# Performance work log

Measured on AMD Instinct MI355X. Metric: run time of the kernel, lower is better.

Reference implementation:

```python
import jax, jax.numpy as jnp
import numpy as np

EPS = 1e-5

def _layer_norm(x, w, b):
    m = jnp.mean(x, axis=-1, keepdims=True)
    v = jnp.var(x, axis=-1, keepdims=True)
    return (x - m) * jax.lax.rsqrt(v + EPS) * w + b


def setup_inputs() -> dict:
    key = jax.random.key(0)
    ks = jax.random.split(key, 8)
    N, L, c_s, c_z, H, d = 2, 512, 384, 128, 12, 32
    w_scale = 0.05  # keep logits in a numerically sane range
    return {
        "s": jax.random.normal(ks[0], (N, L, c_s), jnp.float32),
        "z": jax.random.normal(ks[1], (N, L, L, c_z), jnp.float32),
        "ln_s_w": jnp.ones((c_s,), jnp.float32),
        "ln_s_b": jnp.zeros((c_s,), jnp.float32),
        "ln_z_w": jnp.ones((c_z,), jnp.float32),
        "ln_z_b": jnp.zeros((c_z,), jnp.float32),
        "wz": jax.random.normal(ks[2], (H, c_z), jnp.float32) * w_scale,
        "wq": jax.random.normal(ks[3], (c_s, H, d), jnp.float32) * w_scale,
        "wk": jax.random.normal(ks[4], (c_s, H, d), jnp.float32) * w_scale,
        "wv": jax.random.normal(ks[5], (c_s, H, d), jnp.float32) * w_scale,
        "wg": jax.random.normal(ks[6], (c_s, H, d), jnp.float32) * w_scale,
        "bg": jnp.ones((H, d), jnp.float32),
        "wo": jax.random.normal(ks[7], (H, d, c_s), jnp.float32) * w_scale,
        "bo": jnp.zeros((c_s,), jnp.float32),
    }


def reference(s, z, ln_s_w, ln_s_b, ln_z_w, ln_z_b, wz, wq, wk, wv, wg, bg, wo, bo):
    d = wq.shape[-1]
    s_n = _layer_norm(s, ln_s_w, ln_s_b)            # [N,L,c_s]
    z_n = _layer_norm(z, ln_z_w, ln_z_b)            # [N,L,L,c_z]
    bias = jnp.einsum('nijc,hc->nhij', z_n, wz)     # [N,H,L,L] per-head pair bias
    q = jnp.einsum('nlc,chd->nhld', s_n, wq) * (1.0 / jnp.sqrt(jnp.asarray(d, s.dtype)))
    k = jnp.einsum('nlc,chd->nhld', s_n, wk)
    v = jnp.einsum('nlc,chd->nhld', s_n, wv)
    logits = jnp.einsum('nhid,nhjd->nhij', q, k) + bias
    attn = jax.nn.softmax(logits, axis=-1)
    o = jnp.einsum('nhij,nhjd->nihd', attn, v)      # [N,L,H,d]
    g = jax.nn.sigmoid(jnp.einsum('nlc,chd->nlhd', s_n, wg) + bg)
    o = o * g
    out = jnp.einsum('nlhd,hdc->nlc', o, wo) + bo   # [N,L,c_s]
    return out
```

## Files before the change

### kernel.cpp

```cpp
#include <hip/hip_runtime.h>
#include <math.h>

#define N_  2
#define L_  512
#define CS  384
#define CZ  128
#define H_  12
#define D_  32
#define HD  384

__device__ __forceinline__ float sigmoidf_(float x) { return 1.f / (1.f + __expf(-x)); }

__global__ __launch_bounds__(64) void k_ln_s(const float* __restrict__ s,
        const float* __restrict__ w, const float* __restrict__ b,
        float* __restrict__ sn) {
    int row = blockIdx.x;
    const float* x = s + (size_t)row * CS;
    float* y = sn + (size_t)row * CS;
    int lane = threadIdx.x;
    float v[6];
    float sum = 0.f, sq = 0.f;
#pragma unroll
    for (int e = 0; e < 6; ++e) {
        v[e] = x[lane + e * 64];
        sum += v[e];
        sq  += v[e] * v[e];
    }
#pragma unroll
    for (int o = 1; o < 64; o <<= 1) {
        sum += __shfl_xor(sum, o);
        sq  += __shfl_xor(sq , o);
    }
    float m = sum * (1.f / CS);
    float var = sq * (1.f / CS) - m * m;
    float rstd = rsqrtf(var + 1e-5f);
#pragma unroll
    for (int e = 0; e < 6; ++e) {
        int c = lane + e * 64;
        y[c] = (v[e] - m) * rstd * w[c] + b[c];
    }
}

__global__ __launch_bounds__(128) void k_wz_prep(const float* __restrict__ lnzw,
        const float* __restrict__ lnzb, const float* __restrict__ wz,
        float* __restrict__ wzp, float* __restrict__ wzps, float* __restrict__ wzb) {
    __shared__ float sp[H_][CZ];
    __shared__ float sb[H_][CZ];
    int c = threadIdx.x;
    float lw = lnzw[c], lb = lnzb[c];
    for (int h = 0; h < H_; ++h) {
        float w = wz[h * CZ + c];
        float p = lw * w;
        sp[h][c] = p;
        sb[h][c] = lb * w;
        wzp[h * CZ + c] = p;
    }
    __syncthreads();
    if (c < H_) {
        float s1 = 0.f, s2 = 0.f;
        for (int e = 0; e < CZ; ++e) { s1 += sp[c][e]; s2 += sb[c][e]; }
        wzps[c] = s1; wzb[c] = s2;
    }
}

__global__ __launch_bounds__(384) void k_proj(const float* __restrict__ sn,
        const float* __restrict__ wq, const float* __restrict__ wk,
        const float* __restrict__ wv, const float* __restrict__ wg,
        float* __restrict__ q, float* __restrict__ k, float* __restrict__ v,
        float* __restrict__ g) {
    __shared__ float s_lds[8][CS];
    int t = threadIdx.x;
    int row0 = blockIdx.x * 8;
    {
        const float4* src = (const float4*)(sn + (size_t)row0 * CS);
        float4* dst = (float4*)(&s_lds[0][0]);
        dst[t] = src[t];
        dst[t + 384] = src[t + 384];
    }
    __syncthreads();
    int mat = t / 96;
    int col = (t % 96) * 4;
    const float* W = (mat == 0) ? wq : (mat == 1) ? wk : (mat == 2) ? wv : wg;
    float acc[8][4];
#pragma unroll
    for (int r = 0; r < 8; ++r)
#pragma unroll
        for (int j = 0; j < 4; ++j) acc[r][j] = 0.f;
    for (int kk = 0; kk < CS; kk += 4) {
        float4 w0 = *(const float4*)(W + (size_t)(kk + 0) * HD + col);
        float4 w1 = *(const float4*)(W + (size_t)(kk + 1) * HD + col);
        float4 w2 = *(const float4*)(W + (size_t)(kk + 2) * HD + col);
        float4 w3 = *(const float4*)(W + (size_t)(kk + 3) * HD + col);
#pragma unroll
        for (int r = 0; r < 8; ++r) {
            float4 sv = *(const float4*)(&s_lds[r][kk]);
            acc[r][0] += sv.x * w0.x + sv.y * w1.x + sv.z * w2.x + sv.w * w3.x;
            acc[r][1] += sv.x * w0.y + sv.y * w1.y + sv.z * w2.y + sv.w * w3.y;
            acc[r][2] += sv.x * w0.z + sv.y * w1.z + sv.z * w2.z + sv.w * w3.z;
            acc[r][3] += sv.x * w0.w + sv.y * w1.w + sv.z * w2.w + sv.w * w3.w;
        }
    }
    float* out = (mat == 0) ? q : (mat == 1) ? k : (mat == 2) ? v : g;
    float scale = (mat == 0) ? 0.17677669529663687f : 1.f;
#pragma unroll
    for (int r = 0; r < 8; ++r) {
        float4 o;
        o.x = acc[r][0] * scale; o.y = acc[r][1] * scale;
        o.z = acc[r][2] * scale; o.w = acc[r][3] * scale;
        *(float4*)(out + (size_t)(row0 + r) * HD + col) = o;
    }
}

__global__ __launch_bounds__(384) void k_bias(const float* __restrict__ z,
        const float* __restrict__ wzp, const float* __restrict__ wzps,
        const float* __restrict__ wzb, float* __restrict__ bias) {
    __shared__ float z_lds[32][132];
    __shared__ float w_lds[H_][132];
    __shared__ float m_lds[32], r_lds[32];
    __shared__ float ws_lds[H_], wb_lds[H_];
    int t = threadIdx.x;
    int jt = blockIdx.x, i = blockIdx.y, n = blockIdx.z;
    int j0 = jt * 32;
    {
        int h = t >> 5, c4 = t & 31;
        *(float4*)(&w_lds[h][c4 * 4]) = *(const float4*)(wzp + h * CZ + c4 * 4);
        if (t < H_) { ws_lds[t] = wzps[t]; wb_lds[t] = wzb[t]; }
    }
    {
        const float4* src = (const float4*)(z + ((size_t)(n * L_ + i) * L_ + j0) * CZ);
        int idx = t;
        *(float4*)(&z_lds[idx >> 5][(idx & 31) * 4]) = src[idx];
        idx = t + 384;
        *(float4*)(&z_lds[idx >> 5][(idx & 31) * 4]) = src[idx];
        if (t < 256) {
            idx = t + 768;
            *(float4*)(&z_lds[idx >> 5][(idx & 31) * 4]) = src[idx];
        }
    }
    __syncthreads();
    if (t < 256) {
        int r = t >> 3, lane = t & 7;
        float s1 = 0.f, s2 = 0.f;
#pragma unroll
        for (int e4 = 0; e4 < 4; ++e4) {
            float4 v = *(const float4*)(&z_lds[r][lane * 16 + e4 * 4]);
            s1 += v.x + v.y + v.z + v.w;
            s2 += v.x * v.x + v.y * v.y + v.z * v.z + v.w * v.w;
        }
#pragma unroll
        for (int o = 1; o < 8; o <<= 1) { s1 += __shfl_xor(s1, o); s2 += __shfl_xor(s2, o); }
        if (lane == 0) {
            float m = s1 * (1.f / CZ);
            float var = s2 * (1.f / CZ) - m * m;
            m_lds[r] = m;
            r_lds[r] = rsqrtf(var + 1e-5f);
        }
    }
    __syncthreads();
    int h = t >> 5, j = t & 31;
    float acc = 0.f;
#pragma unroll 8
    for (int c4 = 0; c4 < 32; ++c4) {
        float4 zv = *(const float4*)(&z_lds[j][c4 * 4]);
        float4 wv = *(const float4*)(&w_lds[h][c4 * 4]);
        acc += zv.x * wv.x + zv.y * wv.y + zv.z * wv.z + zv.w * wv.w;
    }
    float bv = r_lds[j] * (acc - m_lds[j] * ws_lds[h]) + wb_lds[h];
    bias[(((size_t)n * H_ + h) * L_ + i) * L_ + j0 + j] = bv;
}

__global__ __launch_bounds__(256) void k_attn(const float* __restrict__ q,
        const float* __restrict__ k, const float* __restrict__ v,
        const float* __restrict__ gpre, const float* __restrict__ bg,
        const float* __restrict__ bias, float* __restrict__ og) {
    __shared__ float p_lds[16][516];
    __shared__ float k_lds[64][36];
    __shared__ float rinv[16];
    int t = threadIdx.x;
    int it = blockIdx.x, h = blockIdx.y, n = blockIdx.z;
    int i0 = it * 16;
    int i = t >> 4, jsub = t & 15;
    float4 qr[8];
    const float* qrow = q + ((size_t)(n * L_) + i0 + i) * HD + h * D_;
#pragma unroll
    for (int d4 = 0; d4 < 8; ++d4) qr[d4] = *(const float4*)(qrow + d4 * 4);
    const float* bias_row = bias + (((size_t)n * H_ + h) * L_ + i0 + i) * L_;

    for (int s = 0; s < 8; ++s) {
        const float* kbase = k + (size_t)(n * L_ + s * 64) * HD + h * D_;
        {
            int idx = t;
            *(float4*)(&k_lds[idx >> 3][(idx & 7) * 4]) =
                *(const float4*)(kbase + (size_t)(idx >> 3) * HD + (idx & 7) * 4);
            idx = t + 256;
            *(float4*)(&k_lds[idx >> 3][(idx & 7) * 4]) =
                *(const float4*)(kbase + (size_t)(idx >> 3) * HD + (idx & 7) * 4);
        }
        __syncthreads();
        float acc[4];
#pragma unroll
        for (int jj = 0; jj < 4; ++jj) acc[jj] = bias_row[s * 64 + jsub + jj * 16];
#pragma unroll
        for (int d4 = 0; d4 < 8; ++d4) {
            float4 qv = qr[d4];
#pragma unroll
            for (int jj = 0; jj < 4; ++jj) {
                float4 kv = *(const float4*)(&k_lds[jsub + jj * 16][d4 * 4]);
                acc[jj] += qv.x * kv.x + qv.y * kv.y + qv.z * kv.z + qv.w * kv.w;
            }
        }
#pragma unroll
        for (int jj = 0; jj < 4; ++jj) p_lds[i][s * 64 + jsub + jj * 16] = acc[jj];
        __syncthreads();
    }
    {
        float mx = -1e30f;
#pragma unroll
        for (int e = 0; e < 8; ++e) {
            float4 x = *(const float4*)(&p_lds[i][jsub * 32 + e * 4]);
            mx = fmaxf(mx, fmaxf(fmaxf(x.x, x.y), fmaxf(x.z, x.w)));
        }
#pragma unroll
        for (int o = 1; o < 16; o <<= 1) mx = fmaxf(mx, __shfl_xor(mx, o));
        float sum = 0.f;
#pragma unroll
        for (int e = 0; e < 8; ++e) {
            float4 x = *(const float4*)(&p_lds[i][jsub * 32 + e * 4]);
            x.x = __expf(x.x - mx); x.y = __expf(x.y - mx);
            x.z = __expf(x.z - mx); x.w = __expf(x.w - mx);
            *(float4*)(&p_lds[i][jsub * 32 + e * 4]) = x;
            sum += x.x + x.y + x.z + x.w;
        }
#pragma unroll
        for (int o = 1; o < 16; o <<= 1) sum += __shfl_xor(sum, o);
        if (jsub == 0) rinv[i] = 1.f / sum;
    }
    __syncthreads();
    {
        int d = jsub * 2;
        const float* vcol = v + (size_t)(n * L_) * HD + h * D_ + d;
        float o0 = 0.f, o1 = 0.f;
        for (int j = 0; j < L_; ++j) {
            float2 vv = *(const float2*)(vcol + (size_t)j * HD);
            float p = p_lds[i][j];
            o0 += p * vv.x; o1 += p * vv.y;
        }
        float ri = rinv[i];
        o0 *= ri; o1 *= ri;
        size_t gidx = ((size_t)(n * L_) + i0 + i) * HD + h * D_ + d;
        float g0 = sigmoidf_(gpre[gidx]     + bg[h * D_ + d]);
        float g1 = sigmoidf_(gpre[gidx + 1] + bg[h * D_ + d + 1]);
        og[gidx]     = o0 * g0;
        og[gidx + 1] = o1 * g1;
    }
}

__global__ __launch_bounds__(384) void k_out(const float* __restrict__ og,
        const float* __restrict__ wo, const float* __restrict__ bo,
        float* __restrict__ out) {
    __shared__ float o_lds[8][HD];
    int t = threadIdx.x;
    int row0 = blockIdx.x * 8;
    {
        const float4* src = (const float4*)(og + (size_t)row0 * HD);
        float4* dst = (float4*)(&o_lds[0][0]);
        dst[t] = src[t];
        dst[t + 384] = src[t + 384];
    }
    __syncthreads();
    float acc[8];
#pragma unroll
    for (int r = 0; r < 8; ++r) acc[r] = 0.f;
    for (int kk = 0; kk < HD; kk += 4) {
        float w0 = wo[(size_t)(kk + 0) * CS + t];
        float w1 = wo[(size_t)(kk + 1) * CS + t];
        float w2 = wo[(size_t)(kk + 2) * CS + t];
        float w3 = wo[(size_t)(kk + 3) * CS + t];
#pragma unroll
        for (int r = 0; r < 8; ++r) {
            float4 ov = *(const float4*)(&o_lds[r][kk]);
            acc[r] += ov.x * w0 + ov.y * w1 + ov.z * w2 + ov.w * w3;
        }
    }
    float bv = bo[t];
#pragma unroll
    for (int r = 0; r < 8; ++r) out[(size_t)(row0 + r) * CS + t] = acc[r] + bv;
}

extern "C" void kernel_launch(void* const* d_in, const int* in_sizes, int n_in,
                              void* d_out, int out_size, void* d_ws, size_t ws_size,
                              hipStream_t stream) {
    const float* s    = (const float*)d_in[0];
    const float* z    = (const float*)d_in[1];
    const float* lnsw = (const float*)d_in[2];
    const float* lnsb = (const float*)d_in[3];
    const float* lnzw = (const float*)d_in[4];
    const float* lnzb = (const float*)d_in[5];
    const float* wz   = (const float*)d_in[6];
    const float* wq   = (const float*)d_in[7];
    const float* wk   = (const float*)d_in[8];
    const float* wv   = (const float*)d_in[9];
    const float* wg   = (const float*)d_in[10];
    const float* bg   = (const float*)d_in[11];
    const float* wo   = (const float*)d_in[12];
    const float* bo   = (const float*)d_in[13];
    float* out = (float*)d_out;

    float* ws = (float*)d_ws;
    const size_t NL = (size_t)N_ * L_;
    float* sn   = ws;  ws += NL * CS;
    float* q    = ws;  ws += NL * HD;
    float* kk   = ws;  ws += NL * HD;
    float* vv   = ws;  ws += NL * HD;
    float* gpre = ws;  ws += NL * HD;
    float* og   = ws;  ws += NL * HD;
    float* wzp  = ws;  ws += H_ * CZ;
    float* wzps = ws;  ws += 16;
    float* wzb  = ws;  ws += 16;
    float* bias = ws;

    k_ln_s<<<dim3(NL), 64, 0, stream>>>(s, lnsw, lnsb, sn);
    k_wz_prep<<<dim3(1), 128, 0, stream>>>(lnzw, lnzb, wz, wzp, wzps, wzb);
    k_proj<<<dim3(128), 384, 0, stream>>>(sn, wq, wk, wv, wg, q, kk, vv, gpre);
    k_bias<<<dim3(16, 512, 2), 384, 0, stream>>>(z, wzp, wzps, wzb, bias);
    k_attn<<<dim3(32, 12, 2), 256, 0, stream>>>(q, kk, vv, gpre, bg, bias, og);
    k_out<<<dim3(128), 384, 0, stream>>>(og, wo, bo, out);
}
```

Baseline: 584.9 us.

## Restructure attention to wave-per-row with double-buffered K/V tiles; split bias dot

```diff
diff --git a/kernel.cpp b/kernel.cpp
--- a/kernel.cpp
+++ b/kernel.cpp
@@ -157,101 +157,154 @@
         }
     }
     __syncthreads();
-    int h = t >> 5, j = t & 31;
-    float acc = 0.f;
-#pragma unroll 8
-    for (int c4 = 0; c4 < 32; ++c4) {
-        float4 zv = *(const float4*)(&z_lds[j][c4 * 4]);
-        float4 wv = *(const float4*)(&w_lds[h][c4 * 4]);
-        acc += zv.x * wv.x + zv.y * wv.y + zv.z * wv.z + zv.w * wv.w;
-    }
-    float bv = r_lds[j] * (acc - m_lds[j] * ws_lds[h]) + wb_lds[h];
-    bias[(((size_t)n * H_ + h) * L_ + i) * L_ + j0 + j] = bv;
-}
-
-__global__ __launch_bounds__(256) void k_attn(const float* __restrict__ q,
+    int hg = t >> 7;
+    int j  = (t >> 2) & 31;
+    int cs = t & 3;
+    const float* zr = &z_lds[j][cs * 32];
+    const float* wr0 = &w_lds[hg * 4 + 0][cs * 32];
+    const float* wr1 = &w_lds[hg * 4 + 1][cs * 32];
+    const float* wr2 = &w_lds[hg * 4 + 2][cs * 32];
+    const float* wr3 = &w_lds[hg * 4 + 3][cs * 32];
+    float a0 = 0.f, a1 = 0.f, a2 = 0.f, a3 = 0.f;
+#pragma unroll
+    for (int e = 0; e < 8; ++e) {
+        float4 zv = *(const float4*)(zr + e * 4);
+        float4 w0 = *(const float4*)(wr0 + e * 4);
+        float4 w1 = *(const float4*)(wr1 + e * 4);
+        float4 w2 = *(const float4*)(wr2 + e * 4);
+        float4 w3 = *(const float4*)(wr3 + e * 4);
+        a0 += zv.x * w0.x + zv.y * w0.y + zv.z * w0.z + zv.w * w0.w;
+        a1 += zv.x * w1.x + zv.y * w1.y + zv.z * w1.z + zv.w * w1.w;
+        a2 += zv.x * w2.x + zv.y * w2.y + zv.z * w2.z + zv.w * w2.w;
+        a3 += zv.x * w3.x + zv.y * w3.y + zv.z * w3.z + zv.w * w3.w;
+    }
+    a0 += __shfl_xor(a0, 1); a0 += __shfl_xor(a0, 2);
+    a1 += __shfl_xor(a1, 1); a1 += __shfl_xor(a1, 2);
+    a2 += __shfl_xor(a2, 1); a2 += __shfl_xor(a2, 2);
+    a3 += __shfl_xor(a3, 1); a3 += __shfl_xor(a3, 2);
+    float dot = (cs == 0) ? a0 : (cs == 1) ? a1 : (cs == 2) ? a2 : a3;
+    int hh = hg * 4 + cs;
+    float bv = r_lds[j] * (dot - m_lds[j] * ws_lds[hh]) + wb_lds[hh];
+    bias[(((size_t)n * H_ + hh) * L_ + i) * L_ + j0 + j] = bv;
+}
+
+__global__ __launch_bounds__(512) void k_attn(const float* __restrict__ q,
         const float* __restrict__ k, const float* __restrict__ v,
         const float* __restrict__ gpre, const float* __restrict__ bg,
         const float* __restrict__ bias, float* __restrict__ og) {
-    __shared__ float p_lds[16][516];
-    __shared__ float k_lds[64][36];
-    __shared__ float rinv[16];
+    __shared__ float t_lds[2][64][36];
     int t = threadIdx.x;
+    int lane = t & 63;
+    int w = t >> 6;
     int it = blockIdx.x, h = blockIdx.y, n = blockIdx.z;
-    int i0 = it * 16;
-    int i = t >> 4, jsub = t & 15;
+    int i = it * 8 + w;
+    int srow = t >> 3, se = t & 7;
+
+    const float* qrow = q + ((size_t)(n * L_) + i) * HD + h * D_;
     float4 qr[8];
-    const float* qrow = q + ((size_t)(n * L_) + i0 + i) * HD + h * D_;
 #pragma unroll
     for (int d4 = 0; d4 < 8; ++d4) qr[d4] = *(const float4*)(qrow + d4 * 4);
-    const float* bias_row = bias + (((size_t)n * H_ + h) * L_ + i0 + i) * L_;
-
+    const float* brow = bias + (((size_t)n * H_ + h) * L_ + i) * L_;
+    const float* kbase = k + (size_t)(n * L_) * HD + h * D_;
+    const float* vbase = v + (size_t)(n * L_) * HD + h * D_;
+
+    *(float4*)(&t_lds[0][srow][se * 4]) =
+        *(const float4*)(kbase + (size_t)srow * HD + se * 4);
+    __syncthreads();
+    float p[8];
+#pragma unroll
     for (int s = 0; s < 8; ++s) {
-        const float* kbase = k + (size_t)(n * L_ + s * 64) * HD + h * D_;
-        {
-            int idx = t;
-            *(float4*)(&k_lds[idx >> 3][(idx & 7) * 4]) =
-                *(const float4*)(kbase + (size_t)(idx >> 3) * HD + (idx & 7) * 4);
-            idx = t + 256;
-            *(float4*)(&k_lds[idx >> 3][(idx & 7) * 4]) =
-                *(const float4*)(kbase + (size_t)(idx >> 3) * HD + (idx & 7) * 4);
-        }
+        float4 stg;
+        if (s < 7)
+            stg = *(const float4*)(kbase + (size_t)((s + 1) * 64 + srow) * HD + se * 4);
+        float acc = brow[s * 64 + lane];
+        const float* kr = &t_lds[s & 1][lane][0];
+#pragma unroll
+        for (int d4 = 0; d4 < 8; ++d4) {
+            float4 kv = *(const float4*)(kr + d4 * 4);
+            float4 qv = qr[d4];
+            acc += qv.x * kv.x + qv.y * kv.y + qv.z * kv.z + qv.w * kv.w;
+        }
+        p[s] = acc;
+        if (s < 7)
+            *(float4*)(&t_lds[(s + 1) & 1][srow][se * 4]) = stg;
         __syncthreads();
-        float acc[4];
-#pragma unroll
-        for (int jj = 0; jj < 4; ++jj) acc[jj] = bias_row[s * 64 + jsub + jj * 16];
+    }
+    float mx = p[0];
+#pragma unroll
+    for (int s = 1; s < 8; ++s) mx = fmaxf(mx, p[s]);
+#pragma unroll
+    for (int o = 1; o < 64; o <<= 1) mx = fmaxf(mx, __shfl_xor(mx, o));
+    float sum = 0.f;
+#pragma unroll
+    for (int s = 0; s < 8; ++s) { p[s] = __expf(p[s] - mx); sum += p[s]; }
+#pragma unroll
+    for (int o = 1; o < 64; o <<= 1) sum += __shfl_xor(sum, o);
+    float rinv = 1.f / sum;
+
+    float acc[32];
+#pragma unroll
+    for (int d = 0; d < 32; ++d) acc[d] = 0.f;
+    *(float4*)(&t_lds[0][srow][se * 4]) =
+        *(const float4*)(vbase + (size_t)srow * HD + se * 4);
+    __syncthreads();
+#pragma unroll
+    for (int s = 0; s < 8; ++s) {
+        float4 stg;
+        if (s < 7)
+            stg = *(const float4*)(vbase + (size_t)((s + 1) * 64 + srow) * HD + se * 4);
+        float e = p[s];
+        const float* vr = &t_lds[s & 1][lane][0];
 #pragma unroll
         for (int d4 = 0; d4 < 8; ++d4) {
-            float4 qv = qr[d4];
-#pragma unroll
-            for (int jj = 0; jj < 4; ++jj) {
-                float4 kv = *(const float4*)(&k_lds[jsub + jj * 16][d4 * 4]);
-                acc[jj] += qv.x * kv.x + qv.y * kv.y + qv.z * kv.z + qv.w * kv.w;
-            }
-        }
-#pragma unroll
-        for (int jj = 0; jj < 4; ++jj) p_lds[i][s * 64 + jsub + jj * 16] = acc[jj];
+            float4 vv = *(const float4*)(vr + d4 * 4);
+            acc[d4 * 4 + 0] += e * vv.x;
+            acc[d4 * 4 + 1] += e * vv.y;
+            acc[d4 * 4 + 2] += e * vv.z;
+            acc[d4 * 4 + 3] += e * vv.w;
+        }
+        if (s < 7)
+            *(float4*)(&t_lds[(s + 1) & 1][srow][se * 4]) = stg;
         __syncthreads();
     }
-    {
-        float mx = -1e30f;
-#pragma unroll
-        for (int e = 0; e < 8; ++e) {
-            float4 x = *(const float4*)(&p_lds[i][jsub * 32 + e * 4]);
-            mx = fmaxf(mx, fmaxf(fmaxf(x.x, x.y), fmaxf(x.z, x.w)));
-        }
-#pragma unroll
-        for (int o = 1; o < 16; o <<= 1) mx = fmaxf(mx, __shfl_xor(mx, o));
-        float sum = 0.f;
-#pragma unroll
-        for (int e = 0; e < 8; ++e) {
-            float4 x = *(const float4*)(&p_lds[i][jsub * 32 + e * 4]);
-            x.x = __expf(x.x - mx); x.y = __expf(x.y - mx);
-            x.z = __expf(x.z - mx); x.w = __expf(x.w - mx);
-            *(float4*)(&p_lds[i][jsub * 32 + e * 4]) = x;
-            sum += x.x + x.y + x.z + x.w;
-        }
-#pragma unroll
-        for (int o = 1; o < 16; o <<= 1) sum += __shfl_xor(sum, o);
-        if (jsub == 0) rinv[i] = 1.f / sum;
-    }
-    __syncthreads();
-    {
-        int d = jsub * 2;
-        const float* vcol = v + (size_t)(n * L_) * HD + h * D_ + d;
-        float o0 = 0.f, o1 = 0.f;
-        for (int j = 0; j < L_; ++j) {
-            float2 vv = *(const float2*)(vcol + (size_t)j * HD);
-            float p = p_lds[i][j];
-            o0 += p * vv.x; o1 += p * vv.y;
-        }
-        float ri = rinv[i];
-        o0 *= ri; o1 *= ri;
-        size_t gidx = ((size_t)(n * L_) + i0 + i) * HD + h * D_ + d;
-        float g0 = sigmoidf_(gpre[gidx]     + bg[h * D_ + d]);
-        float g1 = sigmoidf_(gpre[gidx + 1] + bg[h * D_ + d + 1]);
-        og[gidx]     = o0 * g0;
-        og[gidx + 1] = o1 * g1;
+    bool b0 = lane & 1, b1 = lane & 2, b2 = lane & 4, b3 = lane & 8, b4 = lane & 16;
+    float r1[16];
+#pragma unroll
+    for (int m = 0; m < 16; ++m) {
+        float give = b0 ? acc[2 * m] : acc[2 * m + 1];
+        float got = __shfl_xor(give, 1);
+        r1[m] = (b0 ? acc[2 * m + 1] : acc[2 * m]) + got;
+    }
+    float r2[8];
+#pragma unroll
+    for (int m = 0; m < 8; ++m) {
+        float give = b1 ? r1[2 * m] : r1[2 * m + 1];
+        float got = __shfl_xor(give, 2);
+        r2[m] = (b1 ? r1[2 * m + 1] : r1[2 * m]) + got;
+    }
+    float r3[4];
+#pragma unroll
+    for (int m = 0; m < 4; ++m) {
+        float give = b2 ? r2[2 * m] : r2[2 * m + 1];
+        float got = __shfl_xor(give, 4);
+        r3[m] = (b2 ? r2[2 * m + 1] : r2[2 * m]) + got;
+    }
+    float r4[2];
+#pragma unroll
+    for (int m = 0; m < 2; ++m) {
+        float give = b3 ? r3[2 * m] : r3[2 * m + 1];
+        float got = __shfl_xor(give, 8);
+        r4[m] = (b3 ? r3[2 * m + 1] : r3[2 * m]) + got;
+    }
+    float give = b4 ? r4[0] : r4[1];
+    float r5 = (b4 ? r4[1] : r4[0]) + __shfl_xor(give, 16);
+    float oval = (r5 + __shfl_xor(r5, 32)) * rinv;
+
+    if (lane < 32) {
+        int d = lane;
+        size_t gi = ((size_t)(n * L_) + i) * HD + h * D_ + d;
+        float g = sigmoidf_(gpre[gi] + bg[h * D_ + d]);
+        og[gi] = oval * g;
     }
 }
 
@@ -323,6 +376,6 @@
     k_wz_prep<<<dim3(1), 128, 0, stream>>>(lnzw, lnzb, wz, wzp, wzps, wzb);
     k_proj<<<dim3(128), 384, 0, stream>>>(sn, wq, wk, wv, wg, q, kk, vv, gpre);
     k_bias<<<dim3(16, 512, 2), 384, 0, stream>>>(z, wzp, wzps, wzb, bias);
-    k_attn<<<dim3(32, 12, 2), 256, 0, stream>>>(q, kk, vv, gpre, bg, bias, og);
+    k_attn<<<dim3(64, 12, 2), 512, 0, stream>>>(q, kk, vv, gpre, bg, bias, og);
     k_out<<<dim3(128), 384, 0, stream>>>(og, wo, bo, out);
 }
```

Result: faster. 543.6 us (-7.1%).
